# Kernel tuning notes

Hardware: AMD Instinct MI355X
Metric: run time of the kernel (lower is better)

## Reference

```python
import jax, jax.numpy as jnp
import numpy as np

B, C, H, W = 64, 64, 64, 64  # C = num_features (time + C-1 space dims)
EPS = 1e-5  # module eps; also used as numerical clamp like the torch manifold


def setup_inputs() -> dict:
    key = jax.random.key(0)
    k1, k2 = jax.random.split(key)
    # Valid Lorentz (k=1) points: x0 = sqrt(1 + ||x_space||^2)
    xs = 0.5 * jax.random.normal(k1, (B, C - 1, H, W), dtype=jnp.float32)
    x0 = jnp.sqrt(1.0 + jnp.sum(xs * xs, axis=1, keepdims=True))
    x = jnp.concatenate([x0, xs], axis=1)  # [B, C, H, W]
    gamma = 0.5 + jax.random.uniform(k2, (C - 1,), dtype=jnp.float32)
    beta = 0.05 * jax.random.normal(jax.random.fold_in(key, 7), (C - 1,), dtype=jnp.float32)
    return {"x": x, "gamma": gamma, "beta": beta}


def reference(x, gamma, beta):
    Bn, Cn, Hn, Wn = x.shape
    xf = x.transpose(0, 2, 3, 1).reshape(-1, Cn)  # [N, C], N = B*H*W

    # Lorentz midpoint (centroid): mean, then normalize by Lorentz norm
    m = jnp.mean(xf, axis=0)                      # [C]
    mm = m[0] * m[0] - jnp.sum(m[1:] * m[1:])     # -<m,m>_L (positive for timelike)
    mu = m / jnp.sqrt(jnp.maximum(mm, EPS))       # [C], on hyperboloid

    # alpha = -<x, mu>_L  (>= 1 on the manifold)
    alpha = xf[:, 0] * mu[0] - xf[:, 1:] @ mu[1:]          # [N]
    alpha = jnp.maximum(alpha, 1.0 + EPS)

    # geodesic distance & Frechet variance
    d = jnp.arccosh(alpha)                                  # [N]
    var = jnp.mean(d * d)

    # logmap at mu: v = d/sqrt(alpha^2-1) * (x - alpha*mu)
    coef = d / jnp.sqrt(alpha * alpha - 1.0)
    v = coef[:, None] * (xf - alpha[:, None] * mu[None, :])  # [N, C]

    # parallel transport mu -> origin o=(1,0,...):
    # PT(v) = v + <o,v>_L/(1 - <mu,o>_L) * (mu + o) = v - v0/(1+mu0) * (mu + o)
    mu_plus_o = mu.at[0].add(1.0)
    vo = v - (v[:, 0] / (1.0 + mu[0]))[:, None] * mu_plus_o[None, :]

    # scale/shift space components, then orthogonal projection back to manifold
    vs = vo[:, 1:]                                           # [N, C-1]
    s = gamma[None, :] * vs / (jnp.sqrt(var) + EPS) + beta[None, :]
    t = jnp.sqrt(1.0 + jnp.sum(s * s, axis=1, keepdims=True))
    out = jnp.concatenate([t, s], axis=1)                    # [N, C]

    return out.reshape(Bn, Hn, Wn, Cn).transpose(0, 3, 1, 2)
```

## Files before the change

### kernel.cpp

```cpp
#include <hip/hip_runtime.h>
#include <math.h>

#define BDIM 64
#define CDIM 64
#define HWN  4096
#define NROWS (BDIM * HWN)
#define CHSTRIDE (CDIM * HWN)
#define EPSV 1e-5f

#define TILE 256
#define ROWBLOCKS (NROWS / TILE)

#define DD_OFF    4096
#define ALPHA_OFF 8192
#define COEF_OFF  (ALPHA_OFF + NROWS)

__global__ __launch_bounds__(256) void k_chansum(const float* __restrict__ x,
                                                 float* __restrict__ ws) {
    const int plane = blockIdx.x;
    const float4* p4 = reinterpret_cast<const float4*>(x + (size_t)plane * HWN);
    float s = 0.f;
#pragma unroll
    for (int i = 0; i < HWN / 4 / 256; ++i) {
        float4 v = p4[threadIdx.x + i * 256];
        s += (v.x + v.y) + (v.z + v.w);
    }
    for (int off = 32; off; off >>= 1) s += __shfl_down(s, off, 64);
    __shared__ float red[4];
    const int lane = threadIdx.x & 63, wid = threadIdx.x >> 6;
    if (lane == 0) red[wid] = s;
    __syncthreads();
    if (threadIdx.x == 0) ws[plane] = (red[0] + red[1]) + (red[2] + red[3]);
}

__device__ __forceinline__ void compute_mu(const float* __restrict__ ws,
                                           float* smu, float* stmp) {
    const int t = threadIdx.x, c = t & 63, g = t >> 6;
    float m = 0.f;
#pragma unroll
    for (int b = 0; b < BDIM / 4; ++b) m += ws[(g * (BDIM / 4) + b) * CDIM + c];
    stmp[g * 64 + c] = m;
    __syncthreads();
    if (t < 64) {
        const float msum = (stmp[c] + stmp[64 + c]) + (stmp[128 + c] + stmp[192 + c]);
        const float mval = msum * (1.0f / (float)NROWS);
        float mm = (c == 0) ? mval * mval : -mval * mval;
        for (int off = 32; off; off >>= 1) mm += __shfl_down(mm, off, 64);
        mm = __shfl(mm, 0, 64);
        smu[c] = mval / sqrtf(fmaxf(mm, EPSV));
    }
    __syncthreads();
}

__device__ __forceinline__ void load_tile(const float* __restrict__ base,
                                          float* __restrict__ tile) {
    const int w = threadIdx.x >> 6, l = threadIdx.x & 63;
#pragma unroll
    for (int s = 0; s < 16; ++s) {
        const int c = s * 4 + w;
        const float4 v = *reinterpret_cast<const float4*>(base + (size_t)c * HWN + 4 * l);
        *reinterpret_cast<float4*>(&tile[c * TILE + 4 * l]) = v;
    }
}

__global__ __launch_bounds__(256) void k_alpha(const float* __restrict__ x,
                                               float* __restrict__ ws) {
    __shared__ float tile[CDIM * TILE];
    __shared__ float smu[64], red[4];
    compute_mu(ws, smu, tile);

    const int n0 = blockIdx.x * TILE;
    const int b = n0 >> 12;
    const int hw0 = n0 & (HWN - 1);
    load_tile(x + (size_t)b * CHSTRIDE + hw0, tile);
    __syncthreads();

    const int t = threadIdx.x;
    float a0 = tile[t] * smu[0]           - tile[TILE + t] * smu[1];
    float a1 = -tile[2 * TILE + t] * smu[2] - tile[3 * TILE + t] * smu[3];
    float a2 = 0.f, a3 = 0.f;
#pragma unroll
    for (int c = 4; c < CDIM; c += 4) {
        a0 -= tile[(c + 0) * TILE + t] * smu[c + 0];
        a1 -= tile[(c + 1) * TILE + t] * smu[c + 1];
        a2 -= tile[(c + 2) * TILE + t] * smu[c + 2];
        a3 -= tile[(c + 3) * TILE + t] * smu[c + 3];
    }
    float alpha = (a0 + a1) + (a2 + a3);
    alpha = fmaxf(alpha, 1.0f + EPSV);
    const float d = acoshf(alpha);
    const float coef = d / sqrtf(alpha * alpha - 1.0f);
    ws[ALPHA_OFF + n0 + t] = alpha;
    ws[COEF_OFF + n0 + t]  = coef;

    float dd = d * d;
    for (int off = 32; off; off >>= 1) dd += __shfl_down(dd, off, 64);
    const int lane = t & 63, wid = t >> 6;
    if (lane == 0) red[wid] = dd;
    __syncthreads();
    if (t == 0) ws[DD_OFF + blockIdx.x] = (red[0] + red[1]) + (red[2] + red[3]);
}

__global__ __launch_bounds__(256) void k_out(const float* __restrict__ x,
                                             const float* __restrict__ gamma,
                                             const float* __restrict__ beta,
                                             float* __restrict__ out,
                                             const float* __restrict__ ws) {
    __shared__ float tile[CDIM * TILE];
    __shared__ float smu[64], sg[64], sb[64], svar[4];
    compute_mu(ws, smu, tile);

    {
        float pd = ws[DD_OFF + threadIdx.x] + ws[DD_OFF + 256 + threadIdx.x] +
                   ws[DD_OFF + 512 + threadIdx.x] + ws[DD_OFF + 768 + threadIdx.x];
        for (int off = 32; off; off >>= 1) pd += __shfl_down(pd, off, 64);
        const int lane = threadIdx.x & 63, wid = threadIdx.x >> 6;
        if (lane == 0) svar[wid] = pd;
        if (threadIdx.x < 64) {
            sg[threadIdx.x] = (threadIdx.x >= 1) ? gamma[threadIdx.x - 1] : 0.f;
            sb[threadIdx.x] = (threadIdx.x >= 1) ? beta[threadIdx.x - 1] : 0.f;
        }
    }
    __syncthreads();
    const float var = ((svar[0] + svar[1]) + (svar[2] + svar[3])) * (1.0f / (float)NROWS);
    const float inv_sv = 1.0f / (sqrtf(var) + EPSV);

    const int n0 = blockIdx.x * TILE;
    const int b = n0 >> 12;
    const int hw0 = n0 & (HWN - 1);
    const size_t gbase = (size_t)b * CHSTRIDE + hw0;
    load_tile(x + gbase, tile);
    __syncthreads();

    const int t = threadIdx.x;
    const float al = ws[ALPHA_OFF + n0 + t];
    const float co = ws[COEF_OFF + n0 + t];
    const float m0 = smu[0];
    const float kk = co * (tile[t] - al * m0) / (1.0f + m0);

    float s2 = 0.f;
#pragma unroll
    for (int c = 1; c < CDIM; ++c) {
        const float xv = tile[c * TILE + t];
        const float m = smu[c];
        const float v = co * (xv - al * m);
        const float vo = v - kk * m;
        const float s = (sg[c] * inv_sv) * vo + sb[c];
        s2 += s * s;
        tile[c * TILE + t] = s;
    }
    tile[t] = sqrtf(1.0f + s2);
    __syncthreads();

    const int w = t >> 6, l = t & 63;
    float* obase = out + gbase;
#pragma unroll
    for (int s = 0; s < 16; ++s) {
        const int c = s * 4 + w;
        const float4 v = *reinterpret_cast<const float4*>(&tile[c * TILE + 4 * l]);
        *reinterpret_cast<float4*>(obase + (size_t)c * HWN + 4 * l) = v;
    }
}

extern "C" void kernel_launch(void* const* d_in, const int* in_sizes, int n_in,
                              void* d_out, int out_size, void* d_ws, size_t ws_size,
                              hipStream_t stream) {
    const float* x     = (const float*)d_in[0];
    const float* gamma = (const float*)d_in[1];
    const float* beta  = (const float*)d_in[2];
    float* out = (float*)d_out;
    float* ws  = (float*)d_ws;

    k_chansum<<<BDIM * CDIM, 256, 0, stream>>>(x, ws);
    k_alpha<<<ROWBLOCKS, 256, 0, stream>>>(x, ws);
    k_out<<<ROWBLOCKS, 256, 0, stream>>>(x, gamma, beta, out, ws);
}
```

Before: 142.5 us.

## Halve row tile, hoist centroid into its own kernel, overlap variance reduce

```diff
diff --git a/kernel.cpp b/kernel.cpp
--- a/kernel.cpp
+++ b/kernel.cpp
@@ -8,10 +8,11 @@
 #define CHSTRIDE (CDIM * HWN)
 #define EPSV 1e-5f
 
-#define TILE 256
+#define TILE 128
 #define ROWBLOCKS (NROWS / TILE)
 
-#define DD_OFF    4096
+#define MU_OFF    4096
+#define DD_OFF    4224
 #define ALPHA_OFF 8192
 #define COEF_OFF  (ALPHA_OFF + NROWS)
 
@@ -33,13 +34,13 @@
     if (threadIdx.x == 0) ws[plane] = (red[0] + red[1]) + (red[2] + red[3]);
 }
 
-__device__ __forceinline__ void compute_mu(const float* __restrict__ ws,
-                                           float* smu, float* stmp) {
+__global__ __launch_bounds__(256) void k_mu(float* __restrict__ ws) {
+    __shared__ float stmp[256];
     const int t = threadIdx.x, c = t & 63, g = t >> 6;
     float m = 0.f;
 #pragma unroll
     for (int b = 0; b < BDIM / 4; ++b) m += ws[(g * (BDIM / 4) + b) * CDIM + c];
-    stmp[g * 64 + c] = m;
+    stmp[t] = m;
     __syncthreads();
     if (t < 64) {
         const float msum = (stmp[c] + stmp[64 + c]) + (stmp[128 + c] + stmp[192 + c]);
@@ -47,27 +48,35 @@
         float mm = (c == 0) ? mval * mval : -mval * mval;
         for (int off = 32; off; off >>= 1) mm += __shfl_down(mm, off, 64);
         mm = __shfl(mm, 0, 64);
-        smu[c] = mval / sqrtf(fmaxf(mm, EPSV));
-    }
-    __syncthreads();
-}
-
-__device__ __forceinline__ void load_tile(const float* __restrict__ base,
-                                          float* __restrict__ tile) {
-    const int w = threadIdx.x >> 6, l = threadIdx.x & 63;
-#pragma unroll
-    for (int s = 0; s < 16; ++s) {
-        const int c = s * 4 + w;
-        const float4 v = *reinterpret_cast<const float4*>(base + (size_t)c * HWN + 4 * l);
-        *reinterpret_cast<float4*>(&tile[c * TILE + 4 * l]) = v;
+        ws[MU_OFF + c] = mval / sqrtf(fmaxf(mm, EPSV));
     }
 }
 
-__global__ __launch_bounds__(256) void k_alpha(const float* __restrict__ x,
+__device__ __forceinline__ float block_reduce128(float v, float* red2) {
+    for (int off = 32; off; off >>= 1) v += __shfl_down(v, off, 64);
+    const int lane = threadIdx.x & 63, w = threadIdx.x >> 6;
+    if (lane == 0) red2[w] = v;
+    __syncthreads();
+    return red2[0] + red2[1];
+}
+
+__device__ __forceinline__ void load_tile(const float* __restrict__ gbase,
+                                          float* __restrict__ tile) {
+    const int w = threadIdx.x >> 6, l = threadIdx.x & 63;
+    const int h = l >> 5, j = l & 31;
+#pragma unroll
+    for (int s = 0; s < 16; ++s) {
+        const int c = (w * 16 + s) * 2 + h;
+        const float4 v = *reinterpret_cast<const float4*>(gbase + (size_t)c * HWN + 4 * j);
+        *reinterpret_cast<float4*>(&tile[c * TILE + 4 * j]) = v;
+    }
+}
+
+__global__ __launch_bounds__(128) void k_alpha(const float* __restrict__ x,
                                                float* __restrict__ ws) {
     __shared__ float tile[CDIM * TILE];
-    __shared__ float smu[64], red[4];
-    compute_mu(ws, smu, tile);
+    __shared__ float smu[64], red2[2];
+    if (threadIdx.x < 64) smu[threadIdx.x] = ws[MU_OFF + threadIdx.x];
 
     const int n0 = blockIdx.x * TILE;
     const int b = n0 >> 12;
@@ -76,7 +85,7 @@
     __syncthreads();
 
     const int t = threadIdx.x;
-    float a0 = tile[t] * smu[0]           - tile[TILE + t] * smu[1];
+    float a0 = tile[t] * smu[0]             - tile[TILE + t] * smu[1];
     float a1 = -tile[2 * TILE + t] * smu[2] - tile[3 * TILE + t] * smu[3];
     float a2 = 0.f, a3 = 0.f;
 #pragma unroll
@@ -93,44 +102,36 @@
     ws[ALPHA_OFF + n0 + t] = alpha;
     ws[COEF_OFF + n0 + t]  = coef;
 
-    float dd = d * d;
-    for (int off = 32; off; off >>= 1) dd += __shfl_down(dd, off, 64);
-    const int lane = t & 63, wid = t >> 6;
-    if (lane == 0) red[wid] = dd;
-    __syncthreads();
-    if (t == 0) ws[DD_OFF + blockIdx.x] = (red[0] + red[1]) + (red[2] + red[3]);
+    const float dd = block_reduce128(d * d, red2);
+    if (t == 0) ws[DD_OFF + blockIdx.x] = dd;
 }
 
-__global__ __launch_bounds__(256) void k_out(const float* __restrict__ x,
+__global__ __launch_bounds__(128) void k_out(const float* __restrict__ x,
                                              const float* __restrict__ gamma,
                                              const float* __restrict__ beta,
                                              float* __restrict__ out,
                                              const float* __restrict__ ws) {
     __shared__ float tile[CDIM * TILE];
-    __shared__ float smu[64], sg[64], sb[64], svar[4];
-    compute_mu(ws, smu, tile);
-
-    {
-        float pd = ws[DD_OFF + threadIdx.x] + ws[DD_OFF + 256 + threadIdx.x] +
-                   ws[DD_OFF + 512 + threadIdx.x] + ws[DD_OFF + 768 + threadIdx.x];
-        for (int off = 32; off; off >>= 1) pd += __shfl_down(pd, off, 64);
-        const int lane = threadIdx.x & 63, wid = threadIdx.x >> 6;
-        if (lane == 0) svar[wid] = pd;
-        if (threadIdx.x < 64) {
-            sg[threadIdx.x] = (threadIdx.x >= 1) ? gamma[threadIdx.x - 1] : 0.f;
-            sb[threadIdx.x] = (threadIdx.x >= 1) ? beta[threadIdx.x - 1] : 0.f;
-        }
+    __shared__ float smu[64], sg[64], sb[64], red2[2];
+    if (threadIdx.x < 64) {
+        smu[threadIdx.x] = ws[MU_OFF + threadIdx.x];
+        sg[threadIdx.x] = (threadIdx.x >= 1) ? gamma[threadIdx.x - 1] : 0.f;
+        sb[threadIdx.x] = (threadIdx.x >= 1) ? beta[threadIdx.x - 1] : 0.f;
     }
-    __syncthreads();
-    const float var = ((svar[0] + svar[1]) + (svar[2] + svar[3])) * (1.0f / (float)NROWS);
-    const float inv_sv = 1.0f / (sqrtf(var) + EPSV);
 
     const int n0 = blockIdx.x * TILE;
     const int b = n0 >> 12;
     const int hw0 = n0 & (HWN - 1);
     const size_t gbase = (size_t)b * CHSTRIDE + hw0;
     load_tile(x + gbase, tile);
-    __syncthreads();
+
+    float pv = 0.f;
+#pragma unroll
+    for (int k = 0; k < ROWBLOCKS / TILE; ++k)
+        pv += ws[DD_OFF + threadIdx.x + TILE * k];
+    const float varsum = block_reduce128(pv, red2);
+    const float var = varsum * (1.0f / (float)NROWS);
+    const float inv_sv = 1.0f / (sqrtf(var) + EPSV);
 
     const int t = threadIdx.x;
     const float al = ws[ALPHA_OFF + n0 + t];
@@ -153,12 +154,13 @@
     __syncthreads();
 
     const int w = t >> 6, l = t & 63;
+    const int h = l >> 5, j = l & 31;
     float* obase = out + gbase;
 #pragma unroll
     for (int s = 0; s < 16; ++s) {
-        const int c = s * 4 + w;
-        const float4 v = *reinterpret_cast<const float4*>(&tile[c * TILE + 4 * l]);
-        *reinterpret_cast<float4*>(obase + (size_t)c * HWN + 4 * l) = v;
+        const int c = (w * 16 + s) * 2 + h;
+        const float4 v = *reinterpret_cast<const float4*>(&tile[c * TILE + 4 * j]);
+        *reinterpret_cast<float4*>(obase + (size_t)c * HWN + 4 * j) = v;
     }
 }
 
@@ -172,6 +174,7 @@
     float* ws  = (float*)d_ws;
 
     k_chansum<<<BDIM * CDIM, 256, 0, stream>>>(x, ws);
-    k_alpha<<<ROWBLOCKS, 256, 0, stream>>>(x, ws);
-    k_out<<<ROWBLOCKS, 256, 0, stream>>>(x, gamma, beta, out, ws);
+    k_mu<<<1, 256, 0, stream>>>(ws);
+    k_alpha<<<ROWBLOCKS, 128, 0, stream>>>(x, ws);
+    k_out<<<ROWBLOCKS, 128, 0, stream>>>(x, gamma, beta, out, ws);
 }
```

Measured after the change: 146.3 us. 2.7% more time.
